# Kernel optimization log

Hardware: AMD Instinct MI355X
Metric: run time of the kernel (lower is better)

Reference implementation:

```python
import jax, jax.numpy as jnp
import numpy as np

B, N, F = 4, 4096, 6
N_CENTROIDS, NSAMPLES, RADIUS = 1024, 64, 0.2


def fps(coords, n_c):
    # iterative farthest point sampling, vectorized over batch
    Bb, Nn, _ = coords.shape
    batch = jnp.arange(Bb)
    first = jnp.zeros((Bb,), jnp.int32)
    init_dist = jnp.full((Bb, Nn), 1e9, coords.dtype)

    def step(carry, _):
        dist, last = carry
        p = coords[batch, last]                      # (B,3) last chosen point
        d = jnp.sum((coords - p[:, None, :]) ** 2, -1)
        dist = jnp.minimum(dist, d)
        nxt = jnp.argmax(dist, -1).astype(jnp.int32)
        return (dist, nxt), nxt

    _, rest = jax.lax.scan(step, (init_dist, first), None, length=n_c - 1)
    return jnp.concatenate([first[None, :], rest], 0).T  # (B, n_c)


def ball_query(coords, centroids, radius, s):
    # coords (B,N,3), centroids (B,C,3) -> (B,C,S) neighbor indices
    Nn = coords.shape[1]
    d = jnp.sum((centroids[:, :, None, :] - coords[:, None, :, :]) ** 2, -1)  # (B,C,N)
    idx = jnp.where(d > radius * radius, Nn, jnp.arange(Nn))
    idx = jnp.sort(idx, axis=-1)[..., :s]
    first = idx[..., :1]                              # centroid itself always valid
    return jnp.where(idx == Nn, first, idx)


def tnet(h, w1, w2, w3, f1, f2):
    # h: (B, P, ch) -> (B, ch, ch) transform matrix (T-Net)
    ch = h.shape[-1]
    t = jax.nn.relu(h @ w1)
    t = jax.nn.relu(t @ w2)
    t = jax.nn.relu(t @ w3)
    t = t.max(axis=1)                                 # global max pool over points
    t = jax.nn.relu(t @ f1)
    return (t @ f2).reshape(-1, ch, ch) + jnp.eye(ch, dtype=h.dtype)


def setup_inputs() -> dict:
    key = jax.random.key(0)
    ks = jax.random.split(key, 20)
    sc = 0.02
    p = lambda k, shape: sc * jax.random.normal(k, shape, dtype=jnp.float32)
    return {
        'x': jax.random.normal(ks[0], (B, N, F), dtype=jnp.float32),
        'points': jax.random.uniform(ks[1], (B, N, 3), dtype=jnp.float32),
        # input T-Net (F x F)
        't1_w1': p(ks[2], (F, 64)), 't1_w2': p(ks[3], (64, 128)), 't1_w3': p(ks[4], (128, 256)),
        't1_f1': p(ks[5], (256, 128)), 't1_f2': p(ks[6], (128, F * F)),
        't2_w1': p(ks[7], (64, 64)), 't2_w2': p(ks[8], (64, 128)), 't2_w3': p(ks[9], (128, 256)),
        't2_f1': p(ks[10], (256, 128)), 't2_f2': p(ks[11], (128, 64 * 64)),
        # shared MLP
        'w1': p(ks[12], (F, 64)), 'w2': p(ks[13], (64, 128)), 'w3': p(ks[14], (128, 256)),
    }


def reference(x, points, t1_w1, t1_w2, t1_w3, t1_f1, t1_f2,
              t2_w1, t2_w2, t2_w3, t2_f1, t2_f2, w1, w2, w3):
    idx = fps(points, N_CENTROIDS)                                       # (B,C)
    centroids = jnp.take_along_axis(points, idx[..., None], axis=1)      # (B,C,3)
    gidx = ball_query(points, centroids, RADIUS, NSAMPLES)               # (B,C,S)
    gather = jax.vmap(lambda a, i: a[i])
    g_xyz = gather(points, gidx) - centroids[:, :, None, :]              # (B,C,S,3)
    g_feat = gather(x, gidx)                                             # (B,C,S,F)

    flat = g_feat.reshape(g_feat.shape[0], -1, g_feat.shape[-1])         # (B,C*S,F)
    inT = tnet(flat, t1_w1, t1_w2, t1_w3, t1_f1, t1_f2)                  # (B,F,F)
    h = jnp.einsum('bpc,bcd->bpd', flat, inT)
    h = jax.nn.relu(h @ w1)                                              # (B,C*S,64)
    feT = tnet(h, t2_w1, t2_w2, t2_w3, t2_f1, t2_f2)                     # (B,64,64)
    h = jnp.einsum('bpc,bcd->bpd', h, feT)
    h = jax.nn.relu(h @ w2)
    h = jax.nn.relu(h @ w3)                                              # (B,C*S,256)
    feats = h.reshape(h.shape[0], N_CENTROIDS, NSAMPLES, -1).max(axis=2) # (B,C,256)
    feats = feats.transpose(0, 2, 1)                                     # (B,256,C)
    return centroids, g_xyz.transpose(0, 3, 1, 2), feats, inT, feT
```

## Files before the change

### kernel.cpp

```cpp
#include <hip/hip_runtime.h>

#define Bb 4
#define Np 4096
#define Ff 6
#define NC 1024
#define NSAMP 64
#define NPTS (Bb*Np)
#define R2 ((float)(0.2*0.2))

static __host__ __device__ constexpr size_t alup(size_t x){ return (x + 255) & ~(size_t)255; }
static constexpr size_t OFF_GIDX = 0;
static constexpr size_t SZ_GIDX  = (size_t)Bb*NC*NSAMP*4;
static constexpr size_t OFF_MASK = alup(OFF_GIDX + SZ_GIDX);
static constexpr size_t SZ_MASK  = (size_t)Bb*Np*4;
static constexpr size_t OFF_T1   = OFF_MASK + SZ_MASK;
static constexpr size_t OFF_T2   = OFF_T1 + (size_t)Bb*256*4;
static constexpr size_t ZERO_BYTES = (OFF_T2 + (size_t)Bb*256*4) - OFF_MASK;
static constexpr size_t OFF_INT  = alup(OFF_T2 + (size_t)Bb*256*4);
static constexpr size_t OFF_FET  = alup(OFF_INT + (size_t)Bb*36*4);
static constexpr size_t OFF_XT    = alup(OFF_FET + (size_t)Bb*4096*4);
static constexpr size_t OFF_HW    = alup(OFF_XT + (size_t)6*NPTS*4);
static constexpr size_t OFF_BUF64 = alup(OFF_HW + (size_t)64*NPTS*4);
static constexpr size_t OFF_BUF128= alup(OFF_BUF64 + (size_t)64*NPTS*4);
static constexpr size_t OFF_FINAL = alup(OFF_BUF128 + (size_t)128*NPTS*4);

__device__ __forceinline__ unsigned wave_red_umax(unsigned v)
{
#define DPP_STEP(ctrl) { unsigned t = (unsigned)__builtin_amdgcn_update_dpp((int)v, (int)v, ctrl, 0xF, 0xF, false); v = (t > v) ? t : v; }
    DPP_STEP(0x111)
    DPP_STEP(0x112)
    DPP_STEP(0x114)
    DPP_STEP(0x118)
    DPP_STEP(0x142)
    DPP_STEP(0x143)
#undef DPP_STEP
    return v;
}

template<int CTRL>
__device__ __forceinline__ double dpp_max_f64(double v)
{
    int lo = __double2loint(v), hi = __double2hiint(v);
    int tlo = __builtin_amdgcn_update_dpp(lo, lo, CTRL, 0xF, 0xF, false);
    int thi = __builtin_amdgcn_update_dpp(hi, hi, CTRL, 0xF, 0xF, false);
    return fmax(v, __hiloint2double(thi, tlo));
}

static constexpr int SMEM_BYTES = 84992;

__global__ __launch_bounds__(256) void mega_kernel(const float* __restrict__ points,
                                                   float* __restrict__ out_cent,
                                                   const float* __restrict__ x,
                                                   float* __restrict__ l3pre,
                                                   const float* __restrict__ t1w1,
                                                   const float* __restrict__ t1w2,
                                                   const float* __restrict__ t1w3)
{
    __shared__ __align__(16) char smem[SMEM_BYTES];

    if (blockIdx.x >= Bb) {
        int tb = blockIdx.x - Bb;
        int g0 = tb * 64;
        int t  = threadIdx.x;
        float* s_in  = (float*)(smem);
        float* s_w1  = (float*)(smem + 1536);
        float* s_a1  = (float*)(smem + 3072);
        float* s_wst = (float*)(smem + 19456);
        float* s_a2  = (float*)(smem + 52224);

        for (int i = t; i < 384; i += 256) {
            int pt = i / 6, c = i % 6;
            s_in[c * 64 + pt] = x[(size_t)(g0 + pt) * 6 + c];
        }
        for (int i = t; i < 384; i += 256)  s_w1[i]  = t1w1[i];
        for (int i = t; i < 8192; i += 256) s_wst[i] = t1w2[i];
        __syncthreads();

        int pt = t & 63;
        int grp = t >> 6;
        {
            int c0 = grp * 16;
            float a[16];
#pragma unroll
            for (int i = 0; i < 16; ++i) a[i] = 0.f;
#pragma unroll
            for (int k = 0; k < 6; ++k) {
                float av = s_in[k * 64 + pt];
#pragma unroll
                for (int i = 0; i < 16; ++i) a[i] += av * s_w1[k * 64 + c0 + i];
            }
#pragma unroll
            for (int i = 0; i < 16; ++i) s_a1[(c0 + i) * 64 + pt] = fmaxf(a[i], 0.f);
        }
        __syncthreads();
        {
            int cg = grp * 32;
            float a[32];
#pragma unroll
            for (int i = 0; i < 32; ++i) a[i] = 0.f;
#pragma unroll 2
            for (int k = 0; k < 64; ++k) {
                float av = s_a1[k * 64 + pt];
                const float4* w = (const float4*)&s_wst[k * 128 + cg];
#pragma unroll
                for (int q = 0; q < 8; ++q) {
                    float4 wv = w[q];
                    a[4*q+0] += av * wv.x; a[4*q+1] += av * wv.y;
                    a[4*q+2] += av * wv.z; a[4*q+3] += av * wv.w;
                }
            }
#pragma unroll
            for (int i = 0; i < 32; ++i) s_a2[(cg + i) * 64 + pt] = fmaxf(a[i], 0.f);
        }
        __syncthreads();
        for (int ch0 = 0; ch0 < 256; ch0 += 64) {
            for (int i = t; i < 8192; i += 256)
                s_wst[i] = t1w3[((size_t)(i >> 6) << 8) + ch0 + (i & 63)];
            __syncthreads();
            int cs = grp * 16;
            float a[16];
#pragma unroll
            for (int i = 0; i < 16; ++i) a[i] = 0.f;
#pragma unroll 2
            for (int k = 0; k < 128; ++k) {
                float av = s_a2[k * 64 + pt];
                const float4* w = (const float4*)&s_wst[k * 64 + cs];
#pragma unroll
                for (int q = 0; q < 4; ++q) {
                    float4 wv = w[q];
                    a[4*q+0] += av * wv.x; a[4*q+1] += av * wv.y;
                    a[4*q+2] += av * wv.z; a[4*q+3] += av * wv.w;
                }
            }
#pragma unroll
            for (int i = 0; i < 16; ++i)
                l3pre[(size_t)(ch0 + cs + i) * NPTS + g0 + pt] = a[i];
            __syncthreads();
        }
        return;
    }

    int b = blockIdx.x;
    const float* P = points + (size_t)b * Np * 3;
    int tid  = threadIdx.x;
    int lane = tid & 63;
    int wave = tid >> 6;

    float4* sc   = (float4*)(smem);
    double* swin = (double*)(smem + 65536);

    float px[16], py[16], pz[16];
    double dk[16];
#pragma unroll
    for (int j = 0; j < 16; ++j) {
        int p = tid + (j << 8);
        float xx = P[p*3+0], yy = P[p*3+1], zz = P[p*3+2];
        px[j] = xx; py[j] = yy; pz[j] = zz;
        dk[j] = __hiloint2double(__float_as_int(1000000000.0f), ~p);
        sc[p] = make_float4(xx, yy, zz, 0.f);
    }
    __syncthreads();

    float cx = sc[0].x, cy = sc[0].y, cz = sc[0].z;
    if (tid == 0) {
        out_cent[((size_t)b*NC + 0)*3 + 0] = cx;
        out_cent[((size_t)b*NC + 0)*3 + 1] = cy;
        out_cent[((size_t)b*NC + 0)*3 + 2] = cz;
    }

    for (int s = 1; s < NC; ++s) {
        double k0 = -1.0, k1 = -1.0, k2 = -1.0, k3 = -1.0;
#pragma unroll
        for (int j = 0; j < 16; ++j) {
            float dx = __fsub_rn(px[j], cx);
            float dy = __fsub_rn(py[j], cy);
            float dz = __fsub_rn(pz[j], cz);
            float d  = __fadd_rn(__fadd_rn(__fmul_rn(dx,dx), __fmul_rn(dy,dy)), __fmul_rn(dz,dz));
            float cur = __uint_as_float((unsigned)__double2hiint(dk[j]));
            float nd  = fminf(cur, d);
            dk[j] = __hiloint2double(__float_as_int(nd), __double2loint(dk[j]));
            if      ((j & 3) == 0) k0 = fmax(k0, dk[j]);
            else if ((j & 3) == 1) k1 = fmax(k1, dk[j]);
            else if ((j & 3) == 2) k2 = fmax(k2, dk[j]);
            else                   k3 = fmax(k3, dk[j]);
        }
        double key = fmax(fmax(k0, k1), fmax(k2, k3));
        key = dpp_max_f64<0x111>(key);
        key = dpp_max_f64<0x112>(key);
        key = dpp_max_f64<0x114>(key);
        key = dpp_max_f64<0x118>(key);
        key = dpp_max_f64<0x142>(key);
        key = dpp_max_f64<0x143>(key);
        if (lane == 63) swin[(s & 1) * 4 + wave] = key;
        __syncthreads();

        const double2* sw = (const double2*)&swin[(s & 1) * 4];
        double2 p01 = sw[0], p23 = sw[1];
        double kk = fmax(fmax(p01.x, p01.y), fmax(p23.x, p23.y));
        int widx = ~__double2loint(kk);

        float4 c = sc[widx];
        cx = c.x; cy = c.y; cz = c.z;
        if (tid == 0) {
            out_cent[((size_t)b*NC + s)*3 + 0] = cx;
            out_cent[((size_t)b*NC + s)*3 + 1] = cy;
            out_cent[((size_t)b*NC + s)*3 + 2] = cz;
        }
    }
}

__global__ __launch_bounds__(256) void ballq_kernel(const float* __restrict__ points,
                                                    const float* __restrict__ cent,
                                                    int* __restrict__ gidx,
                                                    int* __restrict__ mask,
                                                    float* __restrict__ out_gxyz)
{
    int gtid = blockIdx.x * 256 + threadIdx.x;
    int wid  = gtid >> 6;
    int lane = threadIdx.x & 63;
    int b = wid >> 10, c = wid & 1023;
    const float* P = points + (size_t)b * Np * 3;
    float cx = cent[((size_t)b*NC + c)*3 + 0];
    float cy = cent[((size_t)b*NC + c)*3 + 1];
    float cz = cent[((size_t)b*NC + c)*3 + 2];

    __shared__ int sidx[4][NSAMP];
    int* my = sidx[threadIdx.x >> 6];

    int count = 0;
    for (int base = 0; base < Np; base += 64) {
        int p = base + lane;
        float dx = __fsub_rn(cx, P[p*3+0]);
        float dy = __fsub_rn(cy, P[p*3+1]);
        float dz = __fsub_rn(cz, P[p*3+2]);
        float d  = __fadd_rn(__fadd_rn(__fmul_rn(dx,dx), __fmul_rn(dy,dy)), __fmul_rn(dz,dz));
        bool inr = !(d > R2);
        unsigned long long mball = __ballot(inr);
        int before = __popcll(mball & ((1ull << lane) - 1ull));
        int pos = count + before;
        if (inr && pos < NSAMP) my[pos] = p;
        count += (int)__popcll(mball);
        if (count >= NSAMP) break;
    }
    __syncthreads();
    int total = count < NSAMP ? count : NSAMP;
    int first = my[0];
    int myi = (lane < total) ? my[lane] : first;
    gidx[(size_t)wid * NSAMP + lane] = myi;
    mask[(size_t)b * Np + myi] = 1;
    float qx = P[myi*3+0], qy = P[myi*3+1], qz = P[myi*3+2];
    out_gxyz[(((size_t)b*3 + 0)*NC + c)*NSAMP + lane] = __fsub_rn(qx, cx);
    out_gxyz[(((size_t)b*3 + 1)*NC + c)*NSAMP + lane] = __fsub_rn(qy, cy);
    out_gxyz[(((size_t)b*3 + 2)*NC + c)*NSAMP + lane] = __fsub_rn(qz, cz);
}

__global__ __launch_bounds__(256) void maxmask_kernel(const float* __restrict__ buf,
                                                      const int* __restrict__ mask,
                                                      float* __restrict__ tmax)
{
    int bid = blockIdx.x;
    int b = bid >> 8, ch = bid & 255;
    int tid = threadIdx.x;
    const float* row = buf + (size_t)ch * NPTS + (size_t)b * Np;
    const int* mk = mask + (size_t)b * Np;
    float m = 0.f;
#pragma unroll
    for (int i = 0; i < Np / 256; ++i) {
        int p = tid + i * 256;
        float v = row[p];
        if (mk[p]) m = fmaxf(m, fmaxf(v, 0.f));
    }
#pragma unroll
    for (int off = 1; off < 64; off <<= 1)
        m = fmaxf(m, __shfl_xor(m, off));
    __shared__ float red[4];
    if ((tid & 63) == 0) red[tid >> 6] = m;
    __syncthreads();
    if (tid == 0) {
        float r = fmaxf(fmaxf(red[0], red[1]), fmaxf(red[2], red[3]));
        tmax[(size_t)b * 256 + ch] = r;
    }
}

template<int K, int N, int NT, bool RELU, bool PM, bool BW, bool TM>
__global__ __launch_bounds__(256) void layer2_k(const float* __restrict__ in,
                                                const float* __restrict__ W,
                                                float* __restrict__ out,
                                                const int* __restrict__ mask,
                                                unsigned* __restrict__ tmax)
{
    static_assert(NT % 4 == 0, "NT multiple of 4");
    int tid = threadIdx.x;
    int g0  = blockIdx.x * 1024 + tid;
    int o0  = blockIdx.y * NT;
    const float* Wb = W;
    if (BW) Wb += (size_t)(blockIdx.x >> 2) * K * N;

    __shared__ __align__(16) float ws[K * NT];
    for (int i = tid; i < K * NT; i += 256)
        ws[i] = Wb[(size_t)(i / NT) * N + o0 + (i % NT)];
    __syncthreads();

    float acc[4][NT];
#pragma unroll
    for (int mi = 0; mi < 4; ++mi)
#pragma unroll
        for (int oo = 0; oo < NT; ++oo) acc[mi][oo] = 0.f;

#pragma unroll 2
    for (int k = 0; k < K; ++k) {
        float a0 = in[(size_t)k * NPTS + g0];
        float a1 = in[(size_t)k * NPTS + g0 + 256];
        float a2 = in[(size_t)k * NPTS + g0 + 512];
        float a3 = in[(size_t)k * NPTS + g0 + 768];
        const float4* wr = (const float4*)&ws[k * NT];
#pragma unroll
        for (int q = 0; q < NT/4; ++q) {
            float4 w = wr[q];
            acc[0][4*q+0] += a0 * w.x;  acc[0][4*q+1] += a0 * w.y;
            acc[0][4*q+2] += a0 * w.z;  acc[0][4*q+3] += a0 * w.w;
            acc[1][4*q+0] += a1 * w.x;  acc[1][4*q+1] += a1 * w.y;
            acc[1][4*q+2] += a1 * w.z;  acc[1][4*q+3] += a1 * w.w;
            acc[2][4*q+0] += a2 * w.x;  acc[2][4*q+1] += a2 * w.y;
            acc[2][4*q+2] += a2 * w.z;  acc[2][4*q+3] += a2 * w.w;
            acc[3][4*q+0] += a3 * w.x;  acc[3][4*q+1] += a3 * w.y;
            acc[3][4*q+2] += a3 * w.z;  acc[3][4*q+3] += a3 * w.w;
        }
    }

    if (TM) {
        float tmv[NT];
#pragma unroll
        for (int oo = 0; oo < NT; ++oo) tmv[oo] = 0.f;
#pragma unroll
        for (int mi = 0; mi < 4; ++mi) {
            bool pres = mask[g0 + mi * 256] != 0;
#pragma unroll
            for (int oo = 0; oo < NT; ++oo) {
                float v = pres ? fmaxf(acc[mi][oo], 0.f) : 0.f;
                tmv[oo] = fmaxf(tmv[oo], v);
            }
        }
        int b = g0 >> 12;
        int lane = tid & 63;
#pragma unroll
        for (int oo = 0; oo < NT; ++oo) {
            unsigned r = wave_red_umax(__float_as_uint(tmv[oo]));
            if (lane == 63)
                atomicMax(&tmax[(b << 8) + o0 + oo], r);
        }
        return;
    }

#pragma unroll
    for (int mi = 0; mi < 4; ++mi) {
        int g = g0 + mi * 256;
#pragma unroll
        for (int oo = 0; oo < NT; ++oo) {
            float v = acc[mi][oo];
            if (RELU) v = fmaxf(v, 0.f);
            if (PM) out[(size_t)g * N + o0 + oo] = v;
            else    out[(size_t)(o0 + oo) * NPTS + g] = v;
        }
    }
}

__global__ __launch_bounds__(256) void l_h_kernel(const float* __restrict__ x,
                                                  const float* __restrict__ t1max,
                                                  const float* __restrict__ f1,
                                                  const float* __restrict__ f2,
                                                  const float* __restrict__ w1,
                                                  float* __restrict__ out_inT,
                                                  float* __restrict__ hw)
{
    int blk = blockIdx.x, t = threadIdx.x;
    int b = blk >> 4;
    __shared__ float tv[256], u[128], sT[36];
    tv[t] = t1max[(size_t)b*256 + t];
    __syncthreads();
    if (t < 128) {
        float acc = 0.f;
        for (int k = 0; k < 256; ++k) acc += tv[k] * f1[(size_t)k*128 + t];
        u[t] = fmaxf(acc, 0.f);
    }
    __syncthreads();
    if (t < 36) {
        float acc = 0.f;
        for (int k = 0; k < 128; ++k) acc += u[k] * f2[(size_t)k*36 + t];
        if (t / 6 == t % 6) acc += 1.0f;
        sT[t] = acc;
        if ((blk & 15) == 0) out_inT[b*36 + t] = acc;
    }
    __syncthreads();

    int g = blk * 256 + t;
    float v[6];
#pragma unroll
    for (int c = 0; c < 6; ++c) v[c] = x[(size_t)g * 6 + c];
    float tt[6];
#pragma unroll
    for (int o = 0; o < 6; ++o) {
        float acc = 0.f;
#pragma unroll
        for (int c = 0; c < 6; ++c) acc += v[c] * sT[c*6 + o];
        tt[o] = acc;
    }
#pragma unroll 8
    for (int j = 0; j < 64; ++j) {
        float acc = 0.f;
#pragma unroll
        for (int o = 0; o < 6; ++o) acc += tt[o] * w1[o*64 + j];
        hw[(size_t)j * NPTS + g] = fmaxf(acc, 0.f);
    }
}

__global__ __launch_bounds__(256) void head2_kernel(const float* __restrict__ t2,
                                                    const float* __restrict__ f1,
                                                    const float* __restrict__ f2,
                                                    float* __restrict__ outT, float* __restrict__ wsT)
{
    int b = blockIdx.x, t = threadIdx.x;
    __shared__ float tv[256], u[128];
    tv[t] = t2[(size_t)b*256 + t];
    __syncthreads();
    if (t < 128) {
        float acc = 0.f;
        for (int k = 0; k < 256; ++k) acc += tv[k] * f1[(size_t)k*128 + t];
        u[t] = fmaxf(acc, 0.f);
    }
    __syncthreads();
    int j = blockIdx.y * 256 + t;
    float acc = 0.f;
#pragma unroll 8
    for (int k = 0; k < 128; ++k) acc += u[k] * f2[(size_t)k*4096 + j];
    if (j / 64 == j % 64) acc += 1.0f;
    outT[(size_t)b*4096 + j] = acc;
    wsT[(size_t)b*4096 + j]  = acc;
}

__global__ __launch_bounds__(256) void feats_kernel(const float* __restrict__ fin,
                                                    const int* __restrict__ gidx,
                                                    float* __restrict__ out)
{
    int bid = blockIdx.x;
    int b = bid >> 10, c = bid & 1023;
    int o = threadIdx.x;
    __shared__ int sid[NSAMP];
    if (o < NSAMP) sid[o] = gidx[(size_t)bid * NSAMP + o];
    __syncthreads();
    const float* fb = fin + (size_t)b * Np * 256;
    float m = -1e30f;
    for (int s = 0; s < NSAMP; ++s)
        m = fmaxf(m, fb[(size_t)sid[s] * 256 + o]);
    out[((size_t)b*256 + o)*NC + c] = m;
}

extern "C" void kernel_launch(void* const* d_in, const int* in_sizes, int n_in,
                              void* d_out, int out_size, void* d_ws, size_t ws_size,
                              hipStream_t stream)
{
    const float* x      = (const float*)d_in[0];
    const float* points = (const float*)d_in[1];
    const float* t1_w1  = (const float*)d_in[2];
    const float* t1_w2  = (const float*)d_in[3];
    const float* t1_w3  = (const float*)d_in[4];
    const float* t1_f1  = (const float*)d_in[5];
    const float* t1_f2  = (const float*)d_in[6];
    const float* t2_w1  = (const float*)d_in[7];
    const float* t2_w2  = (const float*)d_in[8];
    const float* t2_w3  = (const float*)d_in[9];
    const float* t2_f1  = (const float*)d_in[10];
    const float* t2_f2  = (const float*)d_in[11];
    const float* w1     = (const float*)d_in[12];
    const float* w2     = (const float*)d_in[13];
    const float* w3     = (const float*)d_in[14];

    float* out = (float*)d_out;
    float* out_cent  = out;
    float* out_gxyz  = out + 12288;
    float* out_feats = out + 798720;
    float* out_inT   = out + 1847296;
    float* out_feT   = out + 1847440;

    char* ws = (char*)d_ws;
    int*      gidx  = (int*)(ws + OFF_GIDX);
    int*      mask  = (int*)(ws + OFF_MASK);
    float*    t1max = (float*)(ws + OFF_T1);
    unsigned* t2max = (unsigned*)(ws + OFF_T2);
    float*    wsFeT = (float*)(ws + OFF_FET);
    float*    hw    = (float*)(ws + OFF_HW);
    float*    buf64 = (float*)(ws + OFF_BUF64);
    float*    buf128= (float*)(ws + OFF_BUF128);
    float*    fin   = (float*)(ws + OFF_FINAL);

    (void)hipMemsetAsync(ws + OFF_MASK, 0, ZERO_BYTES, stream);

    mega_kernel<<<Bb + 256, 256, 0, stream>>>(points, out_cent, x, fin, t1_w1, t1_w2, t1_w3);
    ballq_kernel<<<(Bb*NC)/4, 256, 0, stream>>>(points, out_cent, gidx, mask, out_gxyz);
    maxmask_kernel<<<Bb*256, 256, 0, stream>>>(fin, mask, t1max);
    l_h_kernel<<<NPTS/256, 256, 0, stream>>>(x, t1max, t1_f1, t1_f2, w1, out_inT, hw);
    layer2_k<64, 64, 16, true,  false, false, false><<<dim3(16, 4), 256, 0, stream>>>(hw,    t2_w1, buf64,  nullptr, nullptr);
    layer2_k<64, 128,16, true,  false, false, false><<<dim3(16, 8), 256, 0, stream>>>(buf64, t2_w2, buf128, nullptr, nullptr);
    layer2_k<128,256,16, false, false, false, true ><<<dim3(16,16), 256, 0, stream>>>(buf128,t2_w3, nullptr, mask, t2max);
    head2_kernel<<<dim3(Bb,16), 256, 0, stream>>>((const float*)t2max, t2_f1, t2_f2, out_feT, wsFeT);
    layer2_k<64, 64, 16, false, false, true,  false><<<dim3(16, 4), 256, 0, stream>>>(hw,    wsFeT, buf64,  nullptr, nullptr);
    layer2_k<64, 128,16, true,  false, false, false><<<dim3(16, 8), 256, 0, stream>>>(buf64, w2,    buf128, nullptr, nullptr);
    layer2_k<128,256,16, true,  true,  false, false><<<dim3(16,16), 256, 0, stream>>>(buf128,w3,    fin,    nullptr, nullptr);
    feats_kernel<<<Bb*NC, 256, 0, stream>>>(fin, gidx, out_feats);

    (void)in_sizes; (void)n_in; (void)out_size; (void)ws_size;
}
```

Before: 758.9 us.

## Fuse per-point MLP chains into two kernels and simplify FPS argmax key

Replaces eight per-layer kernels (the l_h kernel, six layer2_k launches and head2) with two fused kernels. Each block keeps a 64-point tile's intermediate activations in shared memory through all layers, so the buf64/buf128 global round trips and most launch overhead go away. The feature T-Net head is recomputed inside every block rather than once per batch. Separately, the FPS loop now keeps plain float distances, does one float max per thread and builds the packed double argmax key only once per iteration, instead of maintaining 16 packed doubles. The risks are large shared-memory footprints (about 116 KB per block) that limit occupancy, and the redundant head computation in each block.

```diff
diff --git a/kernel.cpp b/kernel.cpp
--- a/kernel.cpp
+++ b/kernel.cpp
@@ -16,13 +16,8 @@
 static constexpr size_t OFF_T1   = OFF_MASK + SZ_MASK;
 static constexpr size_t OFF_T2   = OFF_T1 + (size_t)Bb*256*4;
 static constexpr size_t ZERO_BYTES = (OFF_T2 + (size_t)Bb*256*4) - OFF_MASK;
-static constexpr size_t OFF_INT  = alup(OFF_T2 + (size_t)Bb*256*4);
-static constexpr size_t OFF_FET  = alup(OFF_INT + (size_t)Bb*36*4);
-static constexpr size_t OFF_XT    = alup(OFF_FET + (size_t)Bb*4096*4);
-static constexpr size_t OFF_HW    = alup(OFF_XT + (size_t)6*NPTS*4);
-static constexpr size_t OFF_BUF64 = alup(OFF_HW + (size_t)64*NPTS*4);
-static constexpr size_t OFF_BUF128= alup(OFF_BUF64 + (size_t)64*NPTS*4);
-static constexpr size_t OFF_FINAL = alup(OFF_BUF128 + (size_t)128*NPTS*4);
+static constexpr size_t OFF_HW    = alup(OFF_T2 + (size_t)Bb*256*4);
+static constexpr size_t OFF_FINAL = alup(OFF_HW + (size_t)64*NPTS*4);
 
 __device__ __forceinline__ unsigned wave_red_umax(unsigned v)
 {
@@ -149,14 +144,13 @@
     float4* sc   = (float4*)(smem);
     double* swin = (double*)(smem + 65536);
 
-    float px[16], py[16], pz[16];
-    double dk[16];
+    float px[16], py[16], pz[16], dist[16];
 #pragma unroll
     for (int j = 0; j < 16; ++j) {
         int p = tid + (j << 8);
         float xx = P[p*3+0], yy = P[p*3+1], zz = P[p*3+2];
         px[j] = xx; py[j] = yy; pz[j] = zz;
-        dk[j] = __hiloint2double(__float_as_int(1000000000.0f), ~p);
+        dist[j] = 1000000000.0f;
         sc[p] = make_float4(xx, yy, zz, 0.f);
     }
     __syncthreads();
@@ -169,22 +163,23 @@
     }
 
     for (int s = 1; s < NC; ++s) {
-        double k0 = -1.0, k1 = -1.0, k2 = -1.0, k3 = -1.0;
+        float m = -1.0f;
 #pragma unroll
         for (int j = 0; j < 16; ++j) {
             float dx = __fsub_rn(px[j], cx);
             float dy = __fsub_rn(py[j], cy);
             float dz = __fsub_rn(pz[j], cz);
             float d  = __fadd_rn(__fadd_rn(__fmul_rn(dx,dx), __fmul_rn(dy,dy)), __fmul_rn(dz,dz));
-            float cur = __uint_as_float((unsigned)__double2hiint(dk[j]));
-            float nd  = fminf(cur, d);
-            dk[j] = __hiloint2double(__float_as_int(nd), __double2loint(dk[j]));
-            if      ((j & 3) == 0) k0 = fmax(k0, dk[j]);
-            else if ((j & 3) == 1) k1 = fmax(k1, dk[j]);
-            else if ((j & 3) == 2) k2 = fmax(k2, dk[j]);
-            else                   k3 = fmax(k3, dk[j]);
-        }
-        double key = fmax(fmax(k0, k1), fmax(k2, k3));
+            float nd = fminf(dist[j], d);
+            dist[j] = nd;
+            m = fmaxf(m, nd);
+        }
+        unsigned pj = 0u;
+#pragma unroll
+        for (int j = 15; j >= 0; --j)
+            pj = (dist[j] == m) ? (unsigned)j : pj;
+        unsigned lo = ~((unsigned)tid + (pj << 8));
+        double key = __hiloint2double(__float_as_int(m), (int)lo);
         key = dpp_max_f64<0x111>(key);
         key = dpp_max_f64<0x112>(key);
         key = dpp_max_f64<0x114>(key);
@@ -282,101 +277,45 @@
     }
 }
 
-template<int K, int N, int NT, bool RELU, bool PM, bool BW, bool TM>
-__global__ __launch_bounds__(256) void layer2_k(const float* __restrict__ in,
-                                                const float* __restrict__ W,
-                                                float* __restrict__ out,
-                                                const int* __restrict__ mask,
-                                                unsigned* __restrict__ tmax)
-{
-    static_assert(NT % 4 == 0, "NT multiple of 4");
-    int tid = threadIdx.x;
-    int g0  = blockIdx.x * 1024 + tid;
-    int o0  = blockIdx.y * NT;
-    const float* Wb = W;
-    if (BW) Wb += (size_t)(blockIdx.x >> 2) * K * N;
-
-    __shared__ __align__(16) float ws[K * NT];
-    for (int i = tid; i < K * NT; i += 256)
-        ws[i] = Wb[(size_t)(i / NT) * N + o0 + (i % NT)];
-    __syncthreads();
-
-    float acc[4][NT];
-#pragma unroll
-    for (int mi = 0; mi < 4; ++mi)
-#pragma unroll
-        for (int oo = 0; oo < NT; ++oo) acc[mi][oo] = 0.f;
-
-#pragma unroll 2
-    for (int k = 0; k < K; ++k) {
-        float a0 = in[(size_t)k * NPTS + g0];
-        float a1 = in[(size_t)k * NPTS + g0 + 256];
-        float a2 = in[(size_t)k * NPTS + g0 + 512];
-        float a3 = in[(size_t)k * NPTS + g0 + 768];
-        const float4* wr = (const float4*)&ws[k * NT];
-#pragma unroll
-        for (int q = 0; q < NT/4; ++q) {
-            float4 w = wr[q];
-            acc[0][4*q+0] += a0 * w.x;  acc[0][4*q+1] += a0 * w.y;
-            acc[0][4*q+2] += a0 * w.z;  acc[0][4*q+3] += a0 * w.w;
-            acc[1][4*q+0] += a1 * w.x;  acc[1][4*q+1] += a1 * w.y;
-            acc[1][4*q+2] += a1 * w.z;  acc[1][4*q+3] += a1 * w.w;
-            acc[2][4*q+0] += a2 * w.x;  acc[2][4*q+1] += a2 * w.y;
-            acc[2][4*q+2] += a2 * w.z;  acc[2][4*q+3] += a2 * w.w;
-            acc[3][4*q+0] += a3 * w.x;  acc[3][4*q+1] += a3 * w.y;
-            acc[3][4*q+2] += a3 * w.z;  acc[3][4*q+3] += a3 * w.w;
-        }
-    }
-
-    if (TM) {
-        float tmv[NT];
-#pragma unroll
-        for (int oo = 0; oo < NT; ++oo) tmv[oo] = 0.f;
-#pragma unroll
-        for (int mi = 0; mi < 4; ++mi) {
-            bool pres = mask[g0 + mi * 256] != 0;
-#pragma unroll
-            for (int oo = 0; oo < NT; ++oo) {
-                float v = pres ? fmaxf(acc[mi][oo], 0.f) : 0.f;
-                tmv[oo] = fmaxf(tmv[oo], v);
-            }
-        }
-        int b = g0 >> 12;
-        int lane = tid & 63;
-#pragma unroll
-        for (int oo = 0; oo < NT; ++oo) {
-            unsigned r = wave_red_umax(__float_as_uint(tmv[oo]));
-            if (lane == 63)
-                atomicMax(&tmax[(b << 8) + o0 + oo], r);
-        }
-        return;
-    }
-
-#pragma unroll
-    for (int mi = 0; mi < 4; ++mi) {
-        int g = g0 + mi * 256;
-#pragma unroll
-        for (int oo = 0; oo < NT; ++oo) {
-            float v = acc[mi][oo];
-            if (RELU) v = fmaxf(v, 0.f);
-            if (PM) out[(size_t)g * N + o0 + oo] = v;
-            else    out[(size_t)(o0 + oo) * NPTS + g] = v;
-        }
-    }
-}
-
-__global__ __launch_bounds__(256) void l_h_kernel(const float* __restrict__ x,
-                                                  const float* __restrict__ t1max,
-                                                  const float* __restrict__ f1,
-                                                  const float* __restrict__ f2,
-                                                  const float* __restrict__ w1,
-                                                  float* __restrict__ out_inT,
-                                                  float* __restrict__ hw)
-{
-    int blk = blockIdx.x, t = threadIdx.x;
-    int b = blk >> 4;
-    __shared__ float tv[256], u[128], sT[36];
-    tv[t] = t1max[(size_t)b*256 + t];
+static constexpr int A_SMEM = 118784;
+
+__global__ __launch_bounds__(256) void fused_t2_kernel(const float* __restrict__ x,
+                                                       const float* __restrict__ t1max,
+                                                       const float* __restrict__ f1,
+                                                       const float* __restrict__ f2,
+                                                       const float* __restrict__ w1,
+                                                       const float* __restrict__ t2w1,
+                                                       const float* __restrict__ t2w2,
+                                                       const float* __restrict__ t2w3,
+                                                       const int*   __restrict__ mask,
+                                                       float* __restrict__ out_inT,
+                                                       float* __restrict__ h_g,
+                                                       unsigned* __restrict__ t2max)
+{
+    __shared__ __align__(16) char smem[A_SMEM];
+    float* s_h  = (float*)(smem);
+    float* s_b1 = (float*)(smem + 16384);
+    float* s_b2 = (float*)(smem + 32768);
+    float* s_wA = (float*)(smem + 65536);
+    float* s_wB = (float*)(smem + 81920);
+    float* tv   = (float*)(smem + 114688);
+    float* u    = (float*)(smem + 115712);
+    float* sT   = (float*)(smem + 116224);
+    float* s_x  = (float*)(smem + 116480);
+
+    int tb = blockIdx.x;
+    int b  = tb >> 6;
+    int g0 = tb * 64;
+    int t  = threadIdx.x;
+    int pt = t & 63;
+    int grp = t >> 6;
+
+    tv[t] = t1max[(size_t)b * 256 + t];
+    for (int i = t; i < 384; i += 256) {
+        int p = i / 6, c = i % 6;
+        s_x[c * 64 + p] = x[(size_t)(g0 + p) * 6 + c];
+    }
+    for (int i = t; i < 4096; i += 256) s_wA[i] = t2w1[i];
     __syncthreads();
     if (t < 128) {
         float acc = 0.f;
@@ -389,53 +328,225 @@
         for (int k = 0; k < 128; ++k) acc += u[k] * f2[(size_t)k*36 + t];
         if (t / 6 == t % 6) acc += 1.0f;
         sT[t] = acc;
-        if ((blk & 15) == 0) out_inT[b*36 + t] = acc;
-    }
-    __syncthreads();
-
-    int g = blk * 256 + t;
-    float v[6];
-#pragma unroll
-    for (int c = 0; c < 6; ++c) v[c] = x[(size_t)g * 6 + c];
-    float tt[6];
-#pragma unroll
-    for (int o = 0; o < 6; ++o) {
-        float acc = 0.f;
-#pragma unroll
-        for (int c = 0; c < 6; ++c) acc += v[c] * sT[c*6 + o];
-        tt[o] = acc;
-    }
-#pragma unroll 8
-    for (int j = 0; j < 64; ++j) {
-        float acc = 0.f;
-#pragma unroll
-        for (int o = 0; o < 6; ++o) acc += tt[o] * w1[o*64 + j];
-        hw[(size_t)j * NPTS + g] = fmaxf(acc, 0.f);
-    }
-}
-
-__global__ __launch_bounds__(256) void head2_kernel(const float* __restrict__ t2,
-                                                    const float* __restrict__ f1,
-                                                    const float* __restrict__ f2,
-                                                    float* __restrict__ outT, float* __restrict__ wsT)
-{
-    int b = blockIdx.x, t = threadIdx.x;
-    __shared__ float tv[256], u[128];
-    tv[t] = t2[(size_t)b*256 + t];
+        if ((tb & 63) == 0) out_inT[b*36 + t] = acc;
+    }
+    for (int i = t; i < 8192; i += 256) s_wB[i] = t2w2[i];
+    __syncthreads();
+
+    {
+        float ttv[6];
+#pragma unroll
+        for (int o = 0; o < 6; ++o) {
+            float acc = 0.f;
+#pragma unroll
+            for (int c = 0; c < 6; ++c) acc += s_x[c*64 + pt] * sT[c*6 + o];
+            ttv[o] = acc;
+        }
+        int cg = grp * 16;
+#pragma unroll
+        for (int i = 0; i < 16; ++i) {
+            float acc = 0.f;
+#pragma unroll
+            for (int o = 0; o < 6; ++o) acc += ttv[o] * w1[o*64 + cg + i];
+            float hv = fmaxf(acc, 0.f);
+            s_h[(cg + i) * 64 + pt] = hv;
+            h_g[(size_t)(cg + i) * NPTS + g0 + pt] = hv;
+        }
+    }
+    __syncthreads();
+
+    {
+        int cg = grp * 16;
+        float a[16];
+#pragma unroll
+        for (int i = 0; i < 16; ++i) a[i] = 0.f;
+#pragma unroll 2
+        for (int k = 0; k < 64; ++k) {
+            float av = s_h[k * 64 + pt];
+            const float4* w = (const float4*)&s_wA[k * 64 + cg];
+#pragma unroll
+            for (int q = 0; q < 4; ++q) {
+                float4 wv = w[q];
+                a[4*q+0] += av * wv.x; a[4*q+1] += av * wv.y;
+                a[4*q+2] += av * wv.z; a[4*q+3] += av * wv.w;
+            }
+        }
+#pragma unroll
+        for (int i = 0; i < 16; ++i) s_b1[(cg + i) * 64 + pt] = fmaxf(a[i], 0.f);
+    }
+    __syncthreads();
+
+    {
+        int cg = grp * 32;
+        float a[32];
+#pragma unroll
+        for (int i = 0; i < 32; ++i) a[i] = 0.f;
+#pragma unroll 2
+        for (int k = 0; k < 64; ++k) {
+            float av = s_b1[k * 64 + pt];
+            const float4* w = (const float4*)&s_wB[k * 128 + cg];
+#pragma unroll
+            for (int q = 0; q < 8; ++q) {
+                float4 wv = w[q];
+                a[4*q+0] += av * wv.x; a[4*q+1] += av * wv.y;
+                a[4*q+2] += av * wv.z; a[4*q+3] += av * wv.w;
+            }
+        }
+#pragma unroll
+        for (int i = 0; i < 32; ++i) s_b2[(cg + i) * 64 + pt] = fmaxf(a[i], 0.f);
+    }
+    __syncthreads();
+
+    bool pres = mask[g0 + pt] != 0;
+    for (int ch0 = 0; ch0 < 256; ch0 += 64) {
+        for (int i = t; i < 8192; i += 256)
+            s_wB[i] = t2w3[((size_t)(i >> 6) << 8) + ch0 + (i & 63)];
+        __syncthreads();
+        int cs = grp * 16;
+        float a[16];
+#pragma unroll
+        for (int i = 0; i < 16; ++i) a[i] = 0.f;
+#pragma unroll 2
+        for (int k = 0; k < 128; ++k) {
+            float av = s_b2[k * 64 + pt];
+            const float4* w = (const float4*)&s_wB[k * 64 + cs];
+#pragma unroll
+            for (int q = 0; q < 4; ++q) {
+                float4 wv = w[q];
+                a[4*q+0] += av * wv.x; a[4*q+1] += av * wv.y;
+                a[4*q+2] += av * wv.z; a[4*q+3] += av * wv.w;
+            }
+        }
+#pragma unroll
+        for (int i = 0; i < 16; ++i) {
+            float v = pres ? fmaxf(a[i], 0.f) : 0.f;
+            unsigned r = wave_red_umax(__float_as_uint(v));
+            if ((t & 63) == 63)
+                atomicMax(&t2max[(b << 8) + ch0 + cs + i], r);
+        }
+        __syncthreads();
+    }
+}
+
+static constexpr int B_SMEM = 116224;
+
+__global__ __launch_bounds__(256) void fused_tail_kernel(const unsigned* __restrict__ t2maxu,
+                                                         const float* __restrict__ f1,
+                                                         const float* __restrict__ f2,
+                                                         const float* __restrict__ h_g,
+                                                         const float* __restrict__ w2,
+                                                         const float* __restrict__ w3,
+                                                         float* __restrict__ out_feT,
+                                                         float* __restrict__ final_g)
+{
+    __shared__ __align__(16) char smem[B_SMEM];
+    float* s_h   = (float*)(smem);
+    float* s_hf  = (float*)(smem + 16384);
+    float* s_c1  = (float*)(smem + 32768);
+    float* s_w   = (float*)(smem + 65536);
+    float* s_feT = (float*)(smem + 98304);
+    float* tv    = (float*)(smem + 114688);
+    float* u     = (float*)(smem + 115712);
+
+    int tb = blockIdx.x;
+    int b  = tb >> 6;
+    int g0 = tb * 64;
+    int t  = threadIdx.x;
+    int pt = t & 63;
+    int grp = t >> 6;
+
+    tv[t] = __uint_as_float(t2maxu[(size_t)b * 256 + t]);
+    for (int i = t; i < 4096; i += 256)
+        s_h[i] = h_g[(size_t)(i >> 6) * NPTS + g0 + (i & 63)];
     __syncthreads();
     if (t < 128) {
         float acc = 0.f;
         for (int k = 0; k < 256; ++k) acc += tv[k] * f1[(size_t)k*128 + t];
         u[t] = fmaxf(acc, 0.f);
     }
-    __syncthreads();
-    int j = blockIdx.y * 256 + t;
-    float acc = 0.f;
+    for (int i = t; i < 8192; i += 256) s_w[i] = w2[i];
+    __syncthreads();
+    bool wrT = (tb & 63) == 0;
+#pragma unroll
+    for (int i = 0; i < 16; ++i) {
+        int j = i * 256 + t;
+        float acc = 0.f;
 #pragma unroll 8
-    for (int k = 0; k < 128; ++k) acc += u[k] * f2[(size_t)k*4096 + j];
-    if (j / 64 == j % 64) acc += 1.0f;
-    outT[(size_t)b*4096 + j] = acc;
-    wsT[(size_t)b*4096 + j]  = acc;
+        for (int k = 0; k < 128; ++k) acc += u[k] * f2[(size_t)k*4096 + j];
+        if ((j >> 6) == (j & 63)) acc += 1.0f;
+        s_feT[j] = acc;
+        if (wrT) out_feT[(size_t)b*4096 + j] = acc;
+    }
+    __syncthreads();
+
+    {
+        int cg = grp * 16;
+        float a[16];
+#pragma unroll
+        for (int i = 0; i < 16; ++i) a[i] = 0.f;
+#pragma unroll 2
+        for (int k = 0; k < 64; ++k) {
+            float av = s_h[k * 64 + pt];
+            const float4* w = (const float4*)&s_feT[k * 64 + cg];
+#pragma unroll
+            for (int q = 0; q < 4; ++q) {
+                float4 wv = w[q];
+                a[4*q+0] += av * wv.x; a[4*q+1] += av * wv.y;
+                a[4*q+2] += av * wv.z; a[4*q+3] += av * wv.w;
+            }
+        }
+#pragma unroll
+        for (int i = 0; i < 16; ++i) s_hf[(cg + i) * 64 + pt] = a[i];
+    }
+    __syncthreads();
+
+    {
+        int cg = grp * 32;
+        float a[32];
+#pragma unroll
+        for (int i = 0; i < 32; ++i) a[i] = 0.f;
+#pragma unroll 2
+        for (int k = 0; k < 64; ++k) {
+            float av = s_hf[k * 64 + pt];
+            const float4* w = (const float4*)&s_w[k * 128 + cg];
+#pragma unroll
+            for (int q = 0; q < 8; ++q) {
+                float4 wv = w[q];
+                a[4*q+0] += av * wv.x; a[4*q+1] += av * wv.y;
+                a[4*q+2] += av * wv.z; a[4*q+3] += av * wv.w;
+            }
+        }
+#pragma unroll
+        for (int i = 0; i < 32; ++i) s_c1[(cg + i) * 64 + pt] = fmaxf(a[i], 0.f);
+    }
+    __syncthreads();
+
+    for (int ch0 = 0; ch0 < 256; ch0 += 64) {
+        for (int i = t; i < 8192; i += 256)
+            s_w[i] = w3[((size_t)(i >> 6) << 8) + ch0 + (i & 63)];
+        __syncthreads();
+        int cs = grp * 16;
+        float a[16];
+#pragma unroll
+        for (int i = 0; i < 16; ++i) a[i] = 0.f;
+#pragma unroll 2
+        for (int k = 0; k < 128; ++k) {
+            float av = s_c1[k * 64 + pt];
+            const float4* w = (const float4*)&s_w[k * 64 + cs];
+#pragma unroll
+            for (int q = 0; q < 4; ++q) {
+                float4 wv = w[q];
+                a[4*q+0] += av * wv.x; a[4*q+1] += av * wv.y;
+                a[4*q+2] += av * wv.z; a[4*q+3] += av * wv.w;
+            }
+        }
+        float4* dst = (float4*)&final_g[(size_t)(g0 + pt) * 256 + ch0 + cs];
+#pragma unroll
+        for (int q = 0; q < 4; ++q)
+            dst[q] = make_float4(fmaxf(a[4*q+0],0.f), fmaxf(a[4*q+1],0.f),
+                                 fmaxf(a[4*q+2],0.f), fmaxf(a[4*q+3],0.f));
+        __syncthreads();
+    }
 }
 
 __global__ __launch_bounds__(256) void feats_kernel(const float* __restrict__ fin,
@@ -487,10 +598,7 @@
     int*      mask  = (int*)(ws + OFF_MASK);
     float*    t1max = (float*)(ws + OFF_T1);
     unsigned* t2max = (unsigned*)(ws + OFF_T2);
-    float*    wsFeT = (float*)(ws + OFF_FET);
-    float*    hw    = (float*)(ws + OFF_HW);
-    float*    buf64 = (float*)(ws + OFF_BUF64);
-    float*    buf128= (float*)(ws + OFF_BUF128);
+    float*    h_g   = (float*)(ws + OFF_HW);
     float*    fin   = (float*)(ws + OFF_FINAL);
 
     (void)hipMemsetAsync(ws + OFF_MASK, 0, ZERO_BYTES, stream);
@@ -498,14 +606,11 @@
     mega_kernel<<<Bb + 256, 256, 0, stream>>>(points, out_cent, x, fin, t1_w1, t1_w2, t1_w3);
     ballq_kernel<<<(Bb*NC)/4, 256, 0, stream>>>(points, out_cent, gidx, mask, out_gxyz);
     maxmask_kernel<<<Bb*256, 256, 0, stream>>>(fin, mask, t1max);
-    l_h_kernel<<<NPTS/256, 256, 0, stream>>>(x, t1max, t1_f1, t1_f2, w1, out_inT, hw);
-    layer2_k<64, 64, 16, true,  false, false, false><<<dim3(16, 4), 256, 0, stream>>>(hw,    t2_w1, buf64,  nullptr, nullptr);
-    layer2_k<64, 128,16, true,  false, false, false><<<dim3(16, 8), 256, 0, stream>>>(buf64, t2_w2, buf128, nullptr, nullptr);
-    layer2_k<128,256,16, false, false, false, true ><<<dim3(16,16), 256, 0, stream>>>(buf128,t2_w3, nullptr, mask, t2max);
-    head2_kernel<<<dim3(Bb,16), 256, 0, stream>>>((const float*)t2max, t2_f1, t2_f2, out_feT, wsFeT);
-    layer2_k<64, 64, 16, false, false, true,  false><<<dim3(16, 4), 256, 0, stream>>>(hw,    wsFeT, buf64,  nullptr, nullptr);
-    layer2_k<64, 128,16, true,  false, false, false><<<dim3(16, 8), 256, 0, stream>>>(buf64, w2,    buf128, nullptr, nullptr);
-    layer2_k<128,256,16, true,  true,  false, false><<<dim3(16,16), 256, 0, stream>>>(buf128,w3,    fin,    nullptr, nullptr);
+    fused_t2_kernel<<<256, 256, 0, stream>>>(x, t1max, t1_f1, t1_f2, w1,
+                                             t2_w1, t2_w2, t2_w3, mask,
+                                             out_inT, h_g, t2max);
+    fused_tail_kernel<<<256, 256, 0, stream>>>(t2max, t2_f1, t2_f2, h_g, w2, w3,
+                                               out_feT, fin);
     feats_kernel<<<Bb*NC, 256, 0, stream>>>(fin, gidx, out_feats);
 
     (void)in_sizes; (void)n_in; (void)out_size; (void)ws_size;
```

Measured after the change: 915.8 us. 20.7% more time.
